# Kernel optimization log

Measured on AMD Instinct MI355X. Metric: run time of the kernel, lower is better.

Reference implementation:

```python
import jax, jax.numpy as jnp
import numpy as np

B, T, D, H = 64, 512, 512, 768
FORGET_BIAS = 1.0  # TF BasicLSTMCell default


def setup_inputs() -> dict:
    key = jax.random.key(0)
    k1, k2, k3, k4 = jax.random.split(key, 4)
    seq = jax.random.normal(k1, (B, T, D), dtype=jnp.float32)
    seq_len = jax.random.randint(k2, (B,), 1, T + 1).astype(jnp.int32)
    s = 1.0 / np.sqrt(D + H)
    W_fw = jax.random.uniform(k3, (D + H, 4 * H), jnp.float32, -s, s)
    W_bw = jax.random.uniform(k4, (D + H, 4 * H), jnp.float32, -s, s)
    b_fw = jnp.zeros((4 * H,), jnp.float32)
    b_bw = jnp.zeros((4 * H,), jnp.float32)
    return {"seq": seq, "seq_len": seq_len, "W_fw": W_fw, "b_fw": b_fw,
            "W_bw": W_bw, "b_bw": b_bw}


def _reverse_sequence(x, seq_len):
    # Mirrors tf.reverse_sequence along time axis 1.
    t = jnp.arange(x.shape[1])
    idx = jnp.where(t[None, :] < seq_len[:, None],
                    seq_len[:, None] - 1 - t[None, :], t[None, :])
    return jnp.take_along_axis(x, idx[:, :, None], axis=1)


def _lstm(x, seq_len, W, b):
    # x: [B, T, D]; W: [D+H, 4H] with TF gate order i, j, f, o.
    b_, t_, _ = x.shape
    h_dim = W.shape[1] // 4

    def step(carry, inp):
        c, h = carry
        x_t, t = inp
        gates = jnp.concatenate([x_t, h], axis=-1) @ W + b
        i, j, f, o = jnp.split(gates, 4, axis=-1)
        new_c = c * jax.nn.sigmoid(f + FORGET_BIAS) + jax.nn.sigmoid(i) * jnp.tanh(j)
        new_h = jnp.tanh(new_c) * jax.nn.sigmoid(o)
        mask = (t < seq_len)[:, None]
        c2 = jnp.where(mask, new_c, c)   # state copied through past seq_len
        h2 = jnp.where(mask, new_h, h)
        out = jnp.where(mask, new_h, jnp.zeros_like(new_h))  # dynamic_rnn zeros outputs
        return (c2, h2), out

    init = (jnp.zeros((b_, h_dim), x.dtype), jnp.zeros((b_, h_dim), x.dtype))
    xs = (jnp.swapaxes(x, 0, 1), jnp.arange(t_))
    (c, h), outs = jax.lax.scan(step, init, xs)
    return jnp.swapaxes(outs, 0, 1), h  # [B,T,H], [B,H]


def reference(seq, seq_len, W_fw, b_fw, W_bw, b_bw):
    out_fw, h_fw = _lstm(seq, seq_len, W_fw, b_fw)
    seq_rev = _reverse_sequence(seq, seq_len)
    out_bw_rev, h_bw = _lstm(seq_rev, seq_len, W_bw, b_bw)
    out_bw = _reverse_sequence(out_bw_rev, seq_len)
    outputs = jnp.concatenate([out_fw, out_bw], axis=-1)   # [B,T,2H]
    state_h = jnp.concatenate([h_fw, h_bw], axis=-1)       # [B,2H]
    return outputs, state_h
```

## Files before the change

kernel.cpp:

```cpp
#include <hip/hip_runtime.h>

#define NB 64
#define NT 512
#define ND 512
#define NH 768
#define KTOT 1280
#define NG 3072
#define NROW (NB * NT)
#define NHG 48
#define NCG 192
#define NKS 40

typedef short bf16x8 __attribute__((ext_vector_type(8)));
typedef float f32x4 __attribute__((ext_vector_type(4)));
typedef _Float16 f16x4 __attribute__((ext_vector_type(4)));

__device__ __forceinline__ unsigned short f2b(float f) {
    unsigned int u; __builtin_memcpy(&u, &f, 4);
    u = u + 0x7FFFu + ((u >> 16) & 1u);
    return (unsigned short)(u >> 16);
}
__device__ __forceinline__ float sigmoidf_(float x) { return 1.f / (1.f + __expf(-x)); }
__device__ __forceinline__ float tanhf_(float x) { return 2.f / (1.f + __expf(-2.f * x)) - 1.f; }

__global__ __launch_bounds__(256) void transpose_w(const float* __restrict__ W,
                                                   unsigned short* __restrict__ WTf) {
    __shared__ float tile[64][65];
    int bx = blockIdx.x % (NG / 64);
    int by = blockIdx.x / (NG / 64);
    int cb = bx * 64, kb = by * 64;
    int tid = threadIdx.x;
    {
        int r = tid >> 2;
        int coff = (tid & 3) * 16;
        const float* src = W + (size_t)(kb + r) * NG + cb + coff;
#pragma unroll
        for (int i = 0; i < 16; i += 4) {
            float4 v = *(const float4*)(src + i);
            tile[coff + i][r] = v.x; tile[coff + i + 1][r] = v.y;
            tile[coff + i + 2][r] = v.z; tile[coff + i + 3][r] = v.w;
        }
    }
    __syncthreads();
#pragma unroll
    for (int it = 0; it < 2; ++it) {
        int id = tid + it * 256;
        int ch = id >> 6;
        int l = id & 63;
        int cgi = ch & 3, ksi = ch >> 2;
        int c = cgi * 16 + (l & 15);
        int k = ksi * 32 + ((l >> 4) * 8);
        bf16x8 o;
#pragma unroll
        for (int j = 0; j < 8; ++j) o[j] = (short)f2b(tile[c][k + j]);
        size_t cg = (size_t)(cb / 16) + cgi;
        size_t ks = (size_t)(kb / 32) + ksi;
        *(bf16x8*)(WTf + ((cg * NKS + ks) * 64 + l) * 8) = o;
    }
}

__global__ __launch_bounds__(256) void convert_x(const float* __restrict__ src,
                                                 unsigned short* __restrict__ dst, int n8) {
    int i = blockIdx.x * 256 + threadIdx.x;
    if (i < n8) {
        const float4* s = (const float4*)(src + (size_t)i * 8);
        float4 v0 = s[0], v1 = s[1];
        bf16x8 o;
        o[0] = (short)f2b(v0.x); o[1] = (short)f2b(v0.y);
        o[2] = (short)f2b(v0.z); o[3] = (short)f2b(v0.w);
        o[4] = (short)f2b(v1.x); o[5] = (short)f2b(v1.y);
        o[6] = (short)f2b(v1.z); o[7] = (short)f2b(v1.w);
        *(bf16x8*)(dst + (size_t)i * 8) = o;
    }
}

__global__ __launch_bounds__(256) void gemm_xw(
    const float* __restrict__ seq,
    const unsigned short* __restrict__ WTf,
    const float* __restrict__ b_fw,
    const float* __restrict__ b_bw,
    _Float16* __restrict__ Gx) {
    __shared__ unsigned short Albs[64 * 522];
    int blk = blockIdx.x;
    int dir = blk >> 9;
    int mbi = blk & 511;
    int mb = mbi * 64;
    const float* bias = dir ? b_bw : b_fw;
    int tid = threadIdx.x;
    {
        int r = tid >> 2;
        int c = tid & 3;
        const float* src = seq + (size_t)(mb + r) * ND;
#pragma unroll
        for (int i = 0; i < 16; ++i) {
            int k = c * 8 + i * 32;
            float4 v0 = *(const float4*)(src + k);
            float4 v1 = *(const float4*)(src + k + 4);
            bf16x8 o;
            o[0] = (short)f2b(v0.x); o[1] = (short)f2b(v0.y);
            o[2] = (short)f2b(v0.z); o[3] = (short)f2b(v0.w);
            o[4] = (short)f2b(v1.x); o[5] = (short)f2b(v1.y);
            o[6] = (short)f2b(v1.z); o[7] = (short)f2b(v1.w);
            *(bf16x8*)&Albs[r * 522 + k] = o;
        }
    }
    __syncthreads();
    int lane = tid & 63, wave = tid >> 6;
    int r0 = lane & 15, qq = lane >> 4, q8 = qq * 8;
    _Float16* gbase = Gx + (size_t)(dir * 512 + mbi) * 196608;
#pragma unroll 1
    for (int nc = 0; nc < 12; ++nc) {
        int colbase = wave * NH + nc * 64;
        f32x4 acc[4][4];
#pragma unroll
        for (int nt = 0; nt < 4; ++nt) {
            float bv = bias[colbase + nt * 16 + r0] + (wave == 2 ? 1.0f : 0.0f);
#pragma unroll
            for (int m = 0; m < 4; ++m) {
                acc[m][nt][0] = bv; acc[m][nt][1] = bv;
                acc[m][nt][2] = bv; acc[m][nt][3] = bv;
            }
        }
        const unsigned short* fpre = WTf +
            ((size_t)(dir * NCG + wave * NHG + nc * 4) * NKS) * 512 + (size_t)lane * 8;
#pragma unroll
        for (int ks = 0; ks < 16; ++ks) {
            bf16x8 a[4], bb[4];
#pragma unroll
            for (int m = 0; m < 4; ++m)
                a[m] = *(const bf16x8*)&Albs[(m * 16 + r0) * 522 + ks * 32 + q8];
#pragma unroll
            for (int nt = 0; nt < 4; ++nt)
                bb[nt] = *(const bf16x8*)(fpre + ((size_t)nt * NKS + ks) * 512);
#pragma unroll
            for (int m = 0; m < 4; ++m)
#pragma unroll
                for (int nt = 0; nt < 4; ++nt)
                    acc[m][nt] = __builtin_amdgcn_mfma_f32_16x16x32_bf16(a[m], bb[nt], acc[m][nt], 0, 0, 0);
        }
#pragma unroll
        for (int nt = 0; nt < 4; ++nt) {
#pragma unroll
            for (int m = 0; m < 4; ++m) {
                f16x4 o;
                o[0] = (_Float16)acc[m][nt][0]; o[1] = (_Float16)acc[m][nt][1];
                o[2] = (_Float16)acc[m][nt][2]; o[3] = (_Float16)acc[m][nt][3];
                *(f16x4*)(gbase + (size_t)((((nc * 4 + wave) * 4 + nt) * 4 + m) * 64 + lane) * 4) = o;
            }
        }
    }
}

__global__ __launch_bounds__(256, 1) void lstm_persistent(
    const float* __restrict__ seq,
    const unsigned short* __restrict__ xbf,
    int mode,
    const int* __restrict__ seq_len,
    const unsigned short* __restrict__ WTf,
    const float* __restrict__ bias_fw,
    const float* __restrict__ bias_bw,
    const _Float16* __restrict__ Gx,
    unsigned short* __restrict__ hbufs,
    float* __restrict__ h_final,
    float* __restrict__ out,
    unsigned int* __restrict__ barrier_cnts)
{
    extern __shared__ char smem[];
    unsigned short* Whf = (unsigned short*)smem;
    float* gl = (float*)(smem + 98304);

    int bid = blockIdx.x;
    int hgroup = bid % NHG;
    int bgroup = (bid / NHG) & 1;
    int dir = bid / (2 * NHG);
    int grp = bid / NHG;
    int b0 = bgroup * 32;
    int hbase = hgroup * 16;
    int tid = threadIdx.x;
    int lane = tid & 63;
    int wave = tid >> 6;
    int r0 = lane & 15;
    int qq = lane >> 4;
    int q8 = qq * 8;

    const float* bias = dir ? bias_bw : bias_fw;
    int col = wave * NH + hbase + r0;
    float bv = bias[col] + (wave == 2 ? 1.0f : 0.0f);

    {
#pragma unroll
        for (int i = 0; i < 24; ++i) {
            int g = i / 6;
            int ks = wave + (i % 6) * 4;
            const unsigned short* src = WTf +
                ((size_t)(dir * NCG + g * NHG + hgroup) * NKS + 16 + ks) * 512 + (size_t)lane * 8;
            *(bf16x8*)(Whf + ((size_t)tid + (size_t)i * 256) * 8) = *(const bf16x8*)src;
        }
    }

    int ebl0 = tid >> 4;
    int ehl = tid & 15;
    int hidx = hbase + ehl;
    int Lb[2]; Lb[0] = seq_len[b0 + ebl0]; Lb[1] = seq_len[b0 + ebl0 + 16];
    float c_reg[2] = {0.f, 0.f};
    unsigned short h_reg[2] = {0, 0};
    size_t eoff[2];
#pragma unroll
    for (int it = 0; it < 2; ++it) {
        int bb = b0 + ebl0 + it * 16;
        eoff[it] = ((size_t)((bb >> 4) * 24 + (hidx >> 5)) * 64 +
                    (size_t)(((hidx >> 3) & 3) * 16 + (bb & 15))) * 8 + (hidx & 7);
    }

    f32x4 ax0, ax1;
    float gxv[8];
    int Rlo[8], Roff[8];
    const _Float16* GxK;
    int Lx[2];

    if (mode == 2) {
        size_t K0 = (size_t)dir * 100663296 + (size_t)(hgroup >> 2) * 16384 +
                    (size_t)wave * 4096 + (size_t)(hgroup & 3) * 1024 + (size_t)r0 * 4;
        GxK = Gx + K0;
#pragma unroll
        for (int i = 0; i < 8; ++i) {
            int br = b0 + (i >> 2) * 16 + qq * 4 + (i & 3);
            int L = seq_len[br];
            Rlo[i] = br * NT;
            Roff[i] = dir ? (L - 1) : 0;
        }
    } else {
        Lx[0] = seq_len[b0 + r0];
        Lx[1] = seq_len[b0 + 16 + r0];
    }

    auto gxload = [&](int stepn) {
#pragma unroll
        for (int i = 0; i < 8; ++i) {
            int tn = dir ? (Roff[i] - stepn) : stepn;
            tn = tn < 0 ? 0 : (tn > NT - 1 ? NT - 1 : tn);
            int R = Rlo[i] + tn;
            size_t a = (size_t)(R >> 6) * 196608 +
                       (size_t)(((R >> 4) & 3) * 256 + ((R >> 2) & 3) * 64 + (R & 3));
            gxv[i] = (float)GxK[a];
        }
    };

    const unsigned short* fbx = WTf +
        ((size_t)(dir * NCG + wave * NHG + hgroup) * NKS) * 512 + (size_t)lane * 8;

    auto xwindow = [&](int stepn) {
        ax0[0] = bv; ax0[1] = bv; ax0[2] = bv; ax0[3] = bv;
        ax1 = ax0;
#pragma unroll
        for (int m = 0; m < 2; ++m) {
            int row = b0 + m * 16 + r0;
            int tn = dir ? (Lx[m] - 1 - stepn) : stepn;
            tn = tn < 0 ? 0 : (tn > NT - 1 ? NT - 1 : tn);
#pragma unroll
            for (int ks = 0; ks < 16; ++ks) {
                bf16x8 av;
                if (mode == 1) {
                    av = *(const bf16x8*)(xbf + ((size_t)row * NT + tn) * ND + ks * 32 + q8);
                } else {
                    const float* xr = seq + ((size_t)row * NT + tn) * ND + ks * 32 + q8;
                    float4 v0 = *(const float4*)xr, v1 = *(const float4*)(xr + 4);
                    av[0] = (short)f2b(v0.x); av[1] = (short)f2b(v0.y);
                    av[2] = (short)f2b(v0.z); av[3] = (short)f2b(v0.w);
                    av[4] = (short)f2b(v1.x); av[5] = (short)f2b(v1.y);
                    av[6] = (short)f2b(v1.z); av[7] = (short)f2b(v1.w);
                }
                bf16x8 bx = *(const bf16x8*)(fbx + (size_t)ks * 512);
                if (m == 0) ax0 = __builtin_amdgcn_mfma_f32_16x16x32_bf16(av, bx, ax0, 0, 0, 0);
                else        ax1 = __builtin_amdgcn_mfma_f32_16x16x32_bf16(av, bx, ax1, 0, 0, 0);
            }
        }
    };

    if (mode == 2) gxload(0); else xwindow(0);
    __syncthreads();

    bf16x8 wb[24];
    {
        const unsigned short* wfp = Whf + (size_t)wave * 12288 + (size_t)lane * 8;
#pragma unroll
        for (int ks = 0; ks < 24; ++ks) wb[ks] = *(const bf16x8*)(wfp + ks * 512);
    }

    unsigned int* cnt = barrier_cnts + grp * 64;
    int rb0 = bgroup * 2;

    for (int step = 0; step < NT; ++step) {
        const unsigned long long* hin64 = (const unsigned long long*)
            (hbufs + (size_t)(step % 3) * (2 * NB * NH) + (size_t)dir * NB * NH);
        unsigned short* hout = hbufs + (size_t)((step + 1) % 3) * (2 * NB * NH) + (size_t)dir * NB * NH;

        unsigned long long huA[24], huB[24];
        auto issue = [&](int c, unsigned long long* hu) {
#pragma unroll
            for (int i = 0; i < 6; ++i) {
                int ks = c * 6 + i;
                size_t o0 = ((size_t)(rb0 * 24 + ks) * 64 + lane) * 2;
                size_t o1 = ((size_t)((rb0 + 1) * 24 + ks) * 64 + lane) * 2;
                hu[4 * i]     = __hip_atomic_load(hin64 + o0,     __ATOMIC_RELAXED, __HIP_MEMORY_SCOPE_AGENT);
                hu[4 * i + 1] = __hip_atomic_load(hin64 + o0 + 1, __ATOMIC_RELAXED, __HIP_MEMORY_SCOPE_AGENT);
                hu[4 * i + 2] = __hip_atomic_load(hin64 + o1,     __ATOMIC_RELAXED, __HIP_MEMORY_SCOPE_AGENT);
                hu[4 * i + 3] = __hip_atomic_load(hin64 + o1 + 1, __ATOMIC_RELAXED, __HIP_MEMORY_SCOPE_AGENT);
            }
        };

        f32x4 acc0, acc1;
        if (mode == 2) {
            acc0[0] = gxv[0]; acc0[1] = gxv[1]; acc0[2] = gxv[2]; acc0[3] = gxv[3];
            acc1[0] = gxv[4]; acc1[1] = gxv[5]; acc1[2] = gxv[6]; acc1[3] = gxv[7];
        } else {
            acc0 = ax0; acc1 = ax1;
        }

        auto consume = [&](int c, const unsigned long long* hu) {
#pragma unroll
            for (int i = 0; i < 6; ++i) {
                int ks = c * 6 + i;
                union { unsigned long long u[2]; bf16x8 v; } fa0, fa1;
                fa0.u[0] = hu[4 * i];     fa0.u[1] = hu[4 * i + 1];
                fa1.u[0] = hu[4 * i + 2]; fa1.u[1] = hu[4 * i + 3];
                acc0 = __builtin_amdgcn_mfma_f32_16x16x32_bf16(fa0.v, wb[ks], acc0, 0, 0, 0);
                acc1 = __builtin_amdgcn_mfma_f32_16x16x32_bf16(fa1.v, wb[ks], acc1, 0, 0, 0);
            }
        };

        issue(0, huA);
        issue(1, huB);
        consume(0, huA); issue(2, huA);
        consume(1, huB); issue(3, huB);
        consume(2, huA);
        consume(3, huB);

#pragma unroll
        for (int r = 0; r < 4; ++r) {
            gl[(wave * 32 + qq * 4 + r) * 17 + r0] = acc0[r];
            gl[(wave * 32 + 16 + qq * 4 + r) * 17 + r0] = acc1[r];
        }
        __syncthreads();

#pragma unroll
        for (int it = 0; it < 2; ++it) {
            int bl = ebl0 + it * 16;
            int bb = b0 + bl;
            if (step < Lb[it]) {
                float gi = gl[(0 * 32 + bl) * 17 + ehl];
                float gj = gl[(1 * 32 + bl) * 17 + ehl];
                float gf = gl[(2 * 32 + bl) * 17 + ehl];
                float go = gl[(3 * 32 + bl) * 17 + ehl];
                float nc = c_reg[it] * sigmoidf_(gf) + sigmoidf_(gi) * tanhf_(gj);
                float nh = tanhf_(nc) * sigmoidf_(go);
                c_reg[it] = nc;
                h_reg[it] = f2b(nh);
                if (step == Lb[it] - 1)
                    h_final[((size_t)dir * NB + bb) * NH + hidx] = nh;
                int t_out = dir ? (Lb[it] - 1 - step) : step;
                out[((size_t)bb * NT + t_out) * (2 * NH) + dir * NH + hidx] = nh;
            } else {
                out[((size_t)bb * NT + step) * (2 * NH) + dir * NH + hidx] = 0.f;
            }
            __hip_atomic_store(&hout[eoff[it]], h_reg[it],
                               __ATOMIC_RELAXED, __HIP_MEMORY_SCOPE_AGENT);
        }

        __syncthreads();

        if (tid == 0)
            __hip_atomic_fetch_add(cnt, 1u, __ATOMIC_RELEASE, __HIP_MEMORY_SCOPE_WORKGROUP);

        if (mode == 2) gxload(step + 1); else xwindow(step + 1);

        if (tid == 0) {
            unsigned int tgt = 48u * (unsigned)(step + 1);
            while (__hip_atomic_load(cnt, __ATOMIC_RELAXED, __HIP_MEMORY_SCOPE_AGENT) < tgt)
                __builtin_amdgcn_s_sleep(2);
        }
        __syncthreads();
    }
}

__global__ __launch_bounds__(256) void write_state(const float* __restrict__ h_final,
                                                   float* __restrict__ out_state) {
    int i = blockIdx.x * 256 + threadIdx.x;
    if (i < 2 * NB * NH) {
        int dir = i / (NB * NH);
        int rem = i - dir * (NB * NH);
        int b = rem / NH, h = rem - (rem / NH) * NH;
        out_state[(size_t)b * (2 * NH) + dir * NH + h] = h_final[i];
    }
}

extern "C" void kernel_launch(void* const* d_in, const int* in_sizes, int n_in,
                              void* d_out, int out_size, void* d_ws, size_t ws_size,
                              hipStream_t stream) {
    const float* seq   = (const float*)d_in[0];
    const int* seq_len = (const int*)d_in[1];
    const float* W_fw  = (const float*)d_in[2];
    const float* b_fw  = (const float*)d_in[3];
    const float* W_bw  = (const float*)d_in[4];
    const float* b_bw  = (const float*)d_in[5];
    float* out = (float*)d_out;

    char* ws = (char*)d_ws;
    size_t off = 0;
    unsigned short* WTf = (unsigned short*)(ws + off); off += (size_t)2 * NG * KTOT * 2;
    unsigned short* hbufs = (unsigned short*)(ws + off);
    size_t hbuf_bytes = (size_t)3 * 2 * NB * NH * 2;   off += hbuf_bytes;
    float* h_final = (float*)(ws + off);
    size_t hf_bytes = (size_t)2 * NB * NH * 4;         off += hf_bytes;
    unsigned int* barrier_cnts = (unsigned int*)(ws + off);
    size_t bar_bytes = 1024;                           off += bar_bytes;

    _Float16* Gx = (_Float16*)(ws + off);
    size_t gx_bytes = (size_t)2 * 512 * 196608 * 2;
    unsigned short* xbf = (unsigned short*)(ws + off);
    size_t xbf_bytes = (size_t)NB * NT * ND * 2;

    int mode = (ws_size >= off + gx_bytes) ? 2
             : ((ws_size >= off + xbf_bytes) ? 1 : 0);

    hipMemsetAsync(hbufs, 0, hbuf_bytes + hf_bytes + bar_bytes, stream);

    transpose_w<<<(KTOT / 64) * (NG / 64), 256, 0, stream>>>(W_fw, WTf);
    transpose_w<<<(KTOT / 64) * (NG / 64), 256, 0, stream>>>(W_bw, WTf + (size_t)NG * KTOT);

    if (mode == 2) {
        gemm_xw<<<1024, 256, 0, stream>>>(seq, WTf, b_fw, b_bw, Gx);
    } else if (mode == 1) {
        int n8 = NB * NT * ND / 8;
        convert_x<<<(n8 + 255) / 256, 256, 0, stream>>>(seq, xbf, n8);
    }

    size_t smem_bytes = 98304 + 8704;
    lstm_persistent<<<192, 256, smem_bytes, stream>>>(
        seq, xbf, mode, seq_len, WTf, b_fw, b_bw, Gx,
        hbufs, h_final, out, barrier_cnts);

    write_state<<<(2 * NB * NH + 255) / 256, 256, 0, stream>>>(
        h_final, out + (size_t)NB * NT * 2 * NH);
}
```

Baseline: 4.063 ms.

## Give each wave all four gates to drop the LDS gate exchange and block syncs

Each block now runs 2 waves, and each wave computes all four gate tiles for its own 16 batch rows. The LSTM cell update can then run straight from the MFMA accumulators, with no LDS gate exchange and no __syncthreads inside the step. Each wave arrives on the cross-block step counter by itself after its h stores drain, and the output and h_final writes move after the arrive so they overlap the barrier wait. In exchange, the recurrent weights are re-read from LDS on every step instead of staying in registers. Each CU also has half as many waves to hide memory latency.

After: 3.696 ms. 1.1x faster.

```diff
diff --git a/kernel.cpp b/kernel.cpp
--- a/kernel.cpp
+++ b/kernel.cpp
@@ -151,7 +151,7 @@
     }
 }
 
-__global__ __launch_bounds__(256, 1) void lstm_persistent(
+__global__ __launch_bounds__(128, 1) void lstm_persistent(
     const float* __restrict__ seq,
     const unsigned short* __restrict__ xbf,
     int mode,
@@ -167,7 +167,6 @@
 {
     extern __shared__ char smem[];
     unsigned short* Whf = (unsigned short*)smem;
-    float* gl = (float*)(smem + 98304);
 
     int bid = blockIdx.x;
     int hgroup = bid % NHG;
@@ -178,101 +177,91 @@
     int hbase = hgroup * 16;
     int tid = threadIdx.x;
     int lane = tid & 63;
-    int wave = tid >> 6;
+    int rh = tid >> 6;
     int r0 = lane & 15;
     int qq = lane >> 4;
-    int q8 = qq * 8;
 
     const float* bias = dir ? bias_bw : bias_fw;
-    int col = wave * NH + hbase + r0;
-    float bv = bias[col] + (wave == 2 ? 1.0f : 0.0f);
-
-    {
-#pragma unroll
-        for (int i = 0; i < 24; ++i) {
-            int g = i / 6;
-            int ks = wave + (i % 6) * 4;
-            const unsigned short* src = WTf +
-                ((size_t)(dir * NCG + g * NHG + hgroup) * NKS + 16 + ks) * 512 + (size_t)lane * 8;
-            *(bf16x8*)(Whf + ((size_t)tid + (size_t)i * 256) * 8) = *(const bf16x8*)src;
-        }
-    }
-
-    int ebl0 = tid >> 4;
-    int ehl = tid & 15;
-    int hidx = hbase + ehl;
-    int Lb[2]; Lb[0] = seq_len[b0 + ebl0]; Lb[1] = seq_len[b0 + ebl0 + 16];
-    float c_reg[2] = {0.f, 0.f};
-    unsigned short h_reg[2] = {0, 0};
-    size_t eoff[2];
-#pragma unroll
-    for (int it = 0; it < 2; ++it) {
-        int bb = b0 + ebl0 + it * 16;
-        eoff[it] = ((size_t)((bb >> 4) * 24 + (hidx >> 5)) * 64 +
-                    (size_t)(((hidx >> 3) & 3) * 16 + (bb & 15))) * 8 + (hidx & 7);
-    }
-
-    f32x4 ax0, ax1;
-    float gxv[8];
-    int Rlo[8], Roff[8];
-    const _Float16* GxK;
-    int Lx[2];
-
+    int hidx = hbase + r0;
+
+#pragma unroll
+    for (int i = 0; i < 48; ++i) {
+        int c = i * 2 + rh;
+        int g = c / 24, ks = c - g * 24;
+        const unsigned short* src = WTf +
+            ((size_t)(dir * NCG + g * NHG + hgroup) * NKS + 16 + ks) * 512 + (size_t)lane * 8;
+        *(bf16x8*)(Whf + ((size_t)c * 64 + lane) * 8) = *(const bf16x8*)src;
+    }
+
+    int rows[4], L[4];
+#pragma unroll
+    for (int e = 0; e < 4; ++e) {
+        rows[e] = b0 + rh * 16 + qq * 4 + e;
+        L[e] = seq_len[rows[e]];
+    }
+    float bvg[4];
+#pragma unroll
+    for (int g = 0; g < 4; ++g) bvg[g] = bias[g * NH + hidx] + (g == 2 ? 1.0f : 0.0f);
+
+    float c_reg[4] = {0.f, 0.f, 0.f, 0.f};
+    unsigned short h_reg[4] = {0, 0, 0, 0};
+    size_t eoff[4];
+#pragma unroll
+    for (int e = 0; e < 4; ++e) {
+        int bb = rows[e];
+        eoff[e] = ((size_t)((bb >> 4) * 24 + (hidx >> 5)) * 64 +
+                   (size_t)(((hidx >> 3) & 3) * 16 + (bb & 15))) * 8 + (hidx & 7);
+    }
+
+    float gxv[16];
+    size_t gK[4];
     if (mode == 2) {
-        size_t K0 = (size_t)dir * 100663296 + (size_t)(hgroup >> 2) * 16384 +
-                    (size_t)wave * 4096 + (size_t)(hgroup & 3) * 1024 + (size_t)r0 * 4;
-        GxK = Gx + K0;
-#pragma unroll
-        for (int i = 0; i < 8; ++i) {
-            int br = b0 + (i >> 2) * 16 + qq * 4 + (i & 3);
-            int L = seq_len[br];
-            Rlo[i] = br * NT;
-            Roff[i] = dir ? (L - 1) : 0;
-        }
-    } else {
-        Lx[0] = seq_len[b0 + r0];
-        Lx[1] = seq_len[b0 + 16 + r0];
-    }
-
+#pragma unroll
+        for (int g = 0; g < 4; ++g)
+            gK[g] = (size_t)dir * 100663296 + (size_t)(hgroup >> 2) * 16384 +
+                    (size_t)g * 4096 + (size_t)(hgroup & 3) * 1024 + (size_t)r0 * 4;
+    }
     auto gxload = [&](int stepn) {
 #pragma unroll
-        for (int i = 0; i < 8; ++i) {
-            int tn = dir ? (Roff[i] - stepn) : stepn;
+        for (int e = 0; e < 4; ++e) {
+            int tn = dir ? (L[e] - 1 - stepn) : stepn;
             tn = tn < 0 ? 0 : (tn > NT - 1 ? NT - 1 : tn);
-            int R = Rlo[i] + tn;
-            size_t a = (size_t)(R >> 6) * 196608 +
-                       (size_t)(((R >> 4) & 3) * 256 + ((R >> 2) & 3) * 64 + (R & 3));
-            gxv[i] = (float)GxK[a];
+            int R = rows[e] * NT + tn;
+            size_t ra = (size_t)(R >> 6) * 196608 +
+                        (size_t)(((R >> 4) & 3) * 256 + ((R >> 2) & 3) * 64 + (R & 3));
+#pragma unroll
+            for (int g = 0; g < 4; ++g) gxv[g * 4 + e] = (float)Gx[gK[g] + ra];
         }
     };
 
-    const unsigned short* fbx = WTf +
-        ((size_t)(dir * NCG + wave * NHG + hgroup) * NKS) * 512 + (size_t)lane * 8;
-
+    f32x4 ax[4];
+    int rowA = b0 + rh * 16 + r0;
+    int LA = seq_len[rowA];
     auto xwindow = [&](int stepn) {
-        ax0[0] = bv; ax0[1] = bv; ax0[2] = bv; ax0[3] = bv;
-        ax1 = ax0;
-#pragma unroll
-        for (int m = 0; m < 2; ++m) {
-            int row = b0 + m * 16 + r0;
-            int tn = dir ? (Lx[m] - 1 - stepn) : stepn;
-            tn = tn < 0 ? 0 : (tn > NT - 1 ? NT - 1 : tn);
-#pragma unroll
-            for (int ks = 0; ks < 16; ++ks) {
-                bf16x8 av;
-                if (mode == 1) {
-                    av = *(const bf16x8*)(xbf + ((size_t)row * NT + tn) * ND + ks * 32 + q8);
-                } else {
-                    const float* xr = seq + ((size_t)row * NT + tn) * ND + ks * 32 + q8;
-                    float4 v0 = *(const float4*)xr, v1 = *(const float4*)(xr + 4);
-                    av[0] = (short)f2b(v0.x); av[1] = (short)f2b(v0.y);
-                    av[2] = (short)f2b(v0.z); av[3] = (short)f2b(v0.w);
-                    av[4] = (short)f2b(v1.x); av[5] = (short)f2b(v1.y);
-                    av[6] = (short)f2b(v1.z); av[7] = (short)f2b(v1.w);
-                }
-                bf16x8 bx = *(const bf16x8*)(fbx + (size_t)ks * 512);
-                if (m == 0) ax0 = __builtin_amdgcn_mfma_f32_16x16x32_bf16(av, bx, ax0, 0, 0, 0);
-                else        ax1 = __builtin_amdgcn_mfma_f32_16x16x32_bf16(av, bx, ax1, 0, 0, 0);
+#pragma unroll
+        for (int g = 0; g < 4; ++g) {
+            ax[g][0] = bvg[g]; ax[g][1] = bvg[g]; ax[g][2] = bvg[g]; ax[g][3] = bvg[g];
+        }
+        int tn = dir ? (LA - 1 - stepn) : stepn;
+        tn = tn < 0 ? 0 : (tn > NT - 1 ? NT - 1 : tn);
+#pragma unroll
+        for (int ks = 0; ks < 16; ++ks) {
+            bf16x8 av;
+            if (mode == 1) {
+                av = *(const bf16x8*)(xbf + ((size_t)rowA * NT + tn) * ND + ks * 32 + qq * 8);
+            } else {
+                const float* xr = seq + ((size_t)rowA * NT + tn) * ND + ks * 32 + qq * 8;
+                float4 v0 = *(const float4*)xr, v1 = *(const float4*)(xr + 4);
+                av[0] = (short)f2b(v0.x); av[1] = (short)f2b(v0.y);
+                av[2] = (short)f2b(v0.z); av[3] = (short)f2b(v0.w);
+                av[4] = (short)f2b(v1.x); av[5] = (short)f2b(v1.y);
+                av[6] = (short)f2b(v1.z); av[7] = (short)f2b(v1.w);
+            }
+#pragma unroll
+            for (int g = 0; g < 4; ++g) {
+                bf16x8 bx = *(const bf16x8*)(WTf +
+                    ((size_t)(dir * NCG + g * NHG + hgroup) * NKS + ks) * 512 + (size_t)lane * 8);
+                ax[g] = __builtin_amdgcn_mfma_f32_16x16x32_bf16(av, bx, ax[g], 0, 0, 0);
             }
         }
     };
@@ -280,52 +269,49 @@
     if (mode == 2) gxload(0); else xwindow(0);
     __syncthreads();
 
-    bf16x8 wb[24];
-    {
-        const unsigned short* wfp = Whf + (size_t)wave * 12288 + (size_t)lane * 8;
-#pragma unroll
-        for (int ks = 0; ks < 24; ++ks) wb[ks] = *(const bf16x8*)(wfp + ks * 512);
-    }
-
     unsigned int* cnt = barrier_cnts + grp * 64;
-    int rb0 = bgroup * 2;
+    int rb = bgroup * 2 + rh;
 
     for (int step = 0; step < NT; ++step) {
         const unsigned long long* hin64 = (const unsigned long long*)
             (hbufs + (size_t)(step % 3) * (2 * NB * NH) + (size_t)dir * NB * NH);
         unsigned short* hout = hbufs + (size_t)((step + 1) % 3) * (2 * NB * NH) + (size_t)dir * NB * NH;
 
-        unsigned long long huA[24], huB[24];
+        unsigned long long huA[12], huB[12];
         auto issue = [&](int c, unsigned long long* hu) {
 #pragma unroll
             for (int i = 0; i < 6; ++i) {
                 int ks = c * 6 + i;
-                size_t o0 = ((size_t)(rb0 * 24 + ks) * 64 + lane) * 2;
-                size_t o1 = ((size_t)((rb0 + 1) * 24 + ks) * 64 + lane) * 2;
-                hu[4 * i]     = __hip_atomic_load(hin64 + o0,     __ATOMIC_RELAXED, __HIP_MEMORY_SCOPE_AGENT);
-                hu[4 * i + 1] = __hip_atomic_load(hin64 + o0 + 1, __ATOMIC_RELAXED, __HIP_MEMORY_SCOPE_AGENT);
-                hu[4 * i + 2] = __hip_atomic_load(hin64 + o1,     __ATOMIC_RELAXED, __HIP_MEMORY_SCOPE_AGENT);
-                hu[4 * i + 3] = __hip_atomic_load(hin64 + o1 + 1, __ATOMIC_RELAXED, __HIP_MEMORY_SCOPE_AGENT);
+                size_t o = ((size_t)(rb * 24 + ks) * 64 + lane) * 2;
+                hu[2 * i]     = __hip_atomic_load(hin64 + o,     __ATOMIC_RELAXED, __HIP_MEMORY_SCOPE_AGENT);
+                hu[2 * i + 1] = __hip_atomic_load(hin64 + o + 1, __ATOMIC_RELAXED, __HIP_MEMORY_SCOPE_AGENT);
             }
         };
 
-        f32x4 acc0, acc1;
+        f32x4 acc[4];
         if (mode == 2) {
-            acc0[0] = gxv[0]; acc0[1] = gxv[1]; acc0[2] = gxv[2]; acc0[3] = gxv[3];
-            acc1[0] = gxv[4]; acc1[1] = gxv[5]; acc1[2] = gxv[6]; acc1[3] = gxv[7];
+#pragma unroll
+            for (int g = 0; g < 4; ++g) {
+                acc[g][0] = gxv[g * 4 + 0]; acc[g][1] = gxv[g * 4 + 1];
+                acc[g][2] = gxv[g * 4 + 2]; acc[g][3] = gxv[g * 4 + 3];
+            }
         } else {
-            acc0 = ax0; acc1 = ax1;
-        }
-
+#pragma unroll
+            for (int g = 0; g < 4; ++g) acc[g] = ax[g];
+        }
+
+        const unsigned short* wf = Whf + (size_t)lane * 8;
         auto consume = [&](int c, const unsigned long long* hu) {
 #pragma unroll
             for (int i = 0; i < 6; ++i) {
                 int ks = c * 6 + i;
-                union { unsigned long long u[2]; bf16x8 v; } fa0, fa1;
-                fa0.u[0] = hu[4 * i];     fa0.u[1] = hu[4 * i + 1];
-                fa1.u[0] = hu[4 * i + 2]; fa1.u[1] = hu[4 * i + 3];
-                acc0 = __builtin_amdgcn_mfma_f32_16x16x32_bf16(fa0.v, wb[ks], acc0, 0, 0, 0);
-                acc1 = __builtin_amdgcn_mfma_f32_16x16x32_bf16(fa1.v, wb[ks], acc1, 0, 0, 0);
+                union { unsigned long long u[2]; bf16x8 v; } fa;
+                fa.u[0] = hu[2 * i]; fa.u[1] = hu[2 * i + 1];
+#pragma unroll
+                for (int g = 0; g < 4; ++g) {
+                    bf16x8 wb = *(const bf16x8*)(wf + (size_t)(g * 24 + ks) * 512);
+                    acc[g] = __builtin_amdgcn_mfma_f32_16x16x32_bf16(fa.v, wb, acc[g], 0, 0, 0);
+                }
             }
         };
 
@@ -336,50 +322,48 @@
         consume(2, huA);
         consume(3, huB);
 
-#pragma unroll
-        for (int r = 0; r < 4; ++r) {
-            gl[(wave * 32 + qq * 4 + r) * 17 + r0] = acc0[r];
-            gl[(wave * 32 + 16 + qq * 4 + r) * 17 + r0] = acc1[r];
-        }
-        __syncthreads();
-
-#pragma unroll
-        for (int it = 0; it < 2; ++it) {
-            int bl = ebl0 + it * 16;
-            int bb = b0 + bl;
-            if (step < Lb[it]) {
-                float gi = gl[(0 * 32 + bl) * 17 + ehl];
-                float gj = gl[(1 * 32 + bl) * 17 + ehl];
-                float gf = gl[(2 * 32 + bl) * 17 + ehl];
-                float go = gl[(3 * 32 + bl) * 17 + ehl];
-                float nc = c_reg[it] * sigmoidf_(gf) + sigmoidf_(gi) * tanhf_(gj);
+        float nhv[4] = {0.f, 0.f, 0.f, 0.f};
+#pragma unroll
+        for (int e = 0; e < 4; ++e) {
+            if (step < L[e]) {
+                float gi = acc[0][e], gj = acc[1][e], gf = acc[2][e], go = acc[3][e];
+                float nc = c_reg[e] * sigmoidf_(gf) + sigmoidf_(gi) * tanhf_(gj);
                 float nh = tanhf_(nc) * sigmoidf_(go);
-                c_reg[it] = nc;
-                h_reg[it] = f2b(nh);
-                if (step == Lb[it] - 1)
-                    h_final[((size_t)dir * NB + bb) * NH + hidx] = nh;
-                int t_out = dir ? (Lb[it] - 1 - step) : step;
-                out[((size_t)bb * NT + t_out) * (2 * NH) + dir * NH + hidx] = nh;
+                c_reg[e] = nc;
+                h_reg[e] = f2b(nh);
+                nhv[e] = nh;
+            }
+            __hip_atomic_store(&hout[eoff[e]], h_reg[e],
+                               __ATOMIC_RELAXED, __HIP_MEMORY_SCOPE_AGENT);
+        }
+
+        asm volatile("s_waitcnt vmcnt(0)" ::: "memory");
+        if (lane == 0)
+            __hip_atomic_fetch_add(cnt, 1u, __ATOMIC_RELEASE, __HIP_MEMORY_SCOPE_WORKGROUP);
+
+        if (mode == 2) gxload(step + 1); else xwindow(step + 1);
+#pragma unroll
+        for (int e = 0; e < 4; ++e) {
+            int bb = rows[e];
+            if (step < L[e]) {
+                int t_out = dir ? (L[e] - 1 - step) : step;
+                out[((size_t)bb * NT + t_out) * (2 * NH) + dir * NH + hidx] = nhv[e];
+                if (step == L[e] - 1)
+                    h_final[((size_t)dir * NB + bb) * NH + hidx] = nhv[e];
             } else {
                 out[((size_t)bb * NT + step) * (2 * NH) + dir * NH + hidx] = 0.f;
             }
-            __hip_atomic_store(&hout[eoff[it]], h_reg[it],
-                               __ATOMIC_RELAXED, __HIP_MEMORY_SCOPE_AGENT);
-        }
-
-        __syncthreads();
-
-        if (tid == 0)
-            __hip_atomic_fetch_add(cnt, 1u, __ATOMIC_RELEASE, __HIP_MEMORY_SCOPE_WORKGROUP);
-
-        if (mode == 2) gxload(step + 1); else xwindow(step + 1);
-
-        if (tid == 0) {
-            unsigned int tgt = 48u * (unsigned)(step + 1);
-            while (__hip_atomic_load(cnt, __ATOMIC_RELAXED, __HIP_MEMORY_SCOPE_AGENT) < tgt)
-                __builtin_amdgcn_s_sleep(2);
-        }
-        __syncthreads();
+        }
+
+        {
+            unsigned int tgt = 96u * (unsigned)(step + 1);
+            if (lane == 0) {
+                while (__hip_atomic_load(cnt, __ATOMIC_RELAXED, __HIP_MEMORY_SCOPE_AGENT) < tgt)
+                    __builtin_amdgcn_s_sleep(2);
+            }
+        }
+        __builtin_amdgcn_sched_barrier(0);
+        asm volatile("" ::: "memory");
     }
 }
 
@@ -435,8 +419,8 @@
         convert_x<<<(n8 + 255) / 256, 256, 0, stream>>>(seq, xbf, n8);
     }
 
-    size_t smem_bytes = 98304 + 8704;
-    lstm_persistent<<<192, 256, smem_bytes, stream>>>(
+    size_t smem_bytes = 98304;
+    lstm_persistent<<<192, 128, smem_bytes, stream>>>(
         seq, xbf, mode, seq_len, WTf, b_fw, b_bw, Gx,
         hbufs, h_final, out, barrier_cnts);
 
```
